# Optimization experiments

Hardware: AMD Instinct MI355X
Metric: run time of the kernel (lower is better)

Reference implementation:

```python
import jax, jax.numpy as jnp
import numpy as np

B, S, D, H = 2, 2048, 1024, 16
HD = D // H          # 64
ROT = HD // 2        # 32

def _rope(x, cos, sin):
    # x: [B,S,H,HD] -> pairs [B,S,H,ROT,2]; cos/sin: [S,ROT] -> [1,S,1,ROT]
    x2 = x.reshape(x.shape[:3] + (ROT, 2))
    x0, x1 = x2[..., 0], x2[..., 1]
    c = cos[None, :, None, :]
    s = sin[None, :, None, :]
    out = jnp.stack([x0 * c - x1 * s, x1 * c + x0 * s], axis=-1)
    return out.reshape(x.shape)

def setup_inputs() -> dict:
    key = jax.random.key(0)
    ks = jax.random.split(key, 5)
    hidden_states = jax.random.normal(ks[0], (B, S, D), dtype=jnp.float32)
    # proper rotary cos/sin table: [S, ROT, 2]
    inv_freq = 1.0 / (10000.0 ** (np.arange(0, ROT, dtype=np.float32) / ROT))
    t = np.arange(S, dtype=np.float32)
    ang = np.outer(t, inv_freq)  # [S, ROT]
    freqs = jnp.asarray(np.stack([np.cos(ang), np.sin(ang)], axis=-1), dtype=jnp.float32)
    sc = 1.0 / np.sqrt(D)
    wq = jax.random.normal(ks[1], (D, D), dtype=jnp.float32) * sc
    wk = jax.random.normal(ks[2], (D, D), dtype=jnp.float32) * sc
    wv = jax.random.normal(ks[3], (D, D), dtype=jnp.float32) * sc
    wo = jax.random.normal(ks[4], (D, D), dtype=jnp.float32) * sc
    return {"hidden_states": hidden_states, "freqs": freqs, "wq": wq, "wk": wk, "wv": wv, "wo": wo}

def reference(hidden_states, freqs, wq, wk, wv, wo):
    b, s, _ = hidden_states.shape
    scaling = HD ** -0.5
    q = (hidden_states @ wq.T).reshape(b, s, H, HD)
    k = (hidden_states @ wk.T).reshape(b, s, H, HD)
    v = (hidden_states @ wv.T).reshape(b, s, H, HD)
    cos, sin = freqs[:s, :, 0], freqs[:s, :, 1]
    q = _rope(q, cos, sin)
    k = _rope(k, cos, sin)
    # [B,H,S,S] scores, fp32 softmax
    scores = jnp.einsum('bqhd,bkhd->bhqk', q, k) * scaling
    attn = jax.nn.softmax(scores.astype(jnp.float32), axis=-1).astype(q.dtype)
    out = jnp.einsum('bhqk,bkhd->bqhd', attn, v).reshape(b, s, D)
    return out @ wo.T
```

## Files before the change

kernel.cpp:

```cpp
#include <hip/hip_runtime.h>
#include <hip/hip_bf16.h>

typedef __attribute__((ext_vector_type(8))) short bf16x8;
typedef __attribute__((ext_vector_type(4))) float f32x4;
typedef __attribute__((ext_vector_type(16))) float f32x16;
typedef __attribute__((ext_vector_type(2))) float f32x2;
typedef unsigned short u16;

#define Bc   2
#define Sc   2048
#define Dc   1024
#define Hc   16
#define HDc  64
#define ROTc 32
#define Mrows 4096

__device__ __forceinline__ u16 f2bf(float x) {
  union { float f; unsigned u; } v{x};
  unsigned r = v.u + 0x7fffu + ((v.u >> 16) & 1u);
  return (u16)(r >> 16);
}
__device__ __forceinline__ float bf2f(u16 x) {
  union { unsigned u; float f; } v{(unsigned)x << 16};
  return v.f;
}
__device__ __forceinline__ unsigned cvtpk(float a, float b) {
  unsigned r;
  asm("v_cvt_pk_bf16_f32 %0, %1, %2" : "=v"(r) : "v"(a), "v"(b));
  return r;
}
__device__ __forceinline__ f32x2 pmax2(f32x2 a, f32x2 b) {
  f32x2 r;
  r.x = fmaxf(a.x, b.x);
  r.y = fmaxf(a.y, b.y);
  return r;
}

__device__ __forceinline__ void gload_lds16(const void* g, void* l) {
  __builtin_amdgcn_global_load_lds(
      (const __attribute__((address_space(1))) void*)g,
      (__attribute__((address_space(3))) void*)l, 16, 0, 0);
}

__global__ void cvt_all(const float* __restrict__ h, const float* __restrict__ q,
                        const float* __restrict__ k, const float* __restrict__ v,
                        const float* __restrict__ o,
                        u16* __restrict__ hb, u16* __restrict__ qb, u16* __restrict__ kb,
                        u16* __restrict__ vb, u16* __restrict__ ob) {
  size_t i = ((size_t)blockIdx.x * 256 + threadIdx.x) * 4;
  const float* s;
  u16* d;
  size_t off;
  if (i < (size_t)Mrows * Dc) {
    s = h; d = hb; off = i;
  } else {
    size_t j = i - (size_t)Mrows * Dc;
    int w = (int)(j >> 20);
    off = j & ((1u << 20) - 1);
    s = (w == 0) ? q : (w == 1) ? k : (w == 2) ? v : o;
    d = (w == 0) ? qb : (w == 1) ? kb : (w == 2) ? vb : ob;
  }
  float4 val = *reinterpret_cast<const float4*>(s + off);
  u16 r0 = f2bf(val.x), r1 = f2bf(val.y), r2 = f2bf(val.z), r3 = f2bf(val.w);
  ushort4 outv = {r0, r1, r2, r3};
  *reinterpret_cast<ushort4*>(d + off) = outv;
}

__global__ void gemm_qkv(const u16* __restrict__ A, const u16* __restrict__ W0,
                         const u16* __restrict__ W1, const u16* __restrict__ W2,
                         const float* __restrict__ freqs,
                         u16* __restrict__ Qo, u16* __restrict__ Ko,
                         u16* __restrict__ Vo) {
  __shared__ u16 As[128 * 32];
  __shared__ u16 Bs[128 * 32];
  const int by = blockIdx.y;
  const int wsel = by >> 3;
  const int n0 = (by & 7) * 128;
  const int m0 = blockIdx.x * 128;
  const u16* Bm = (wsel == 0) ? W0 : (wsel == 1) ? W1 : W2;
  const int t = threadIdx.x;
  const int w = t >> 6;
  const int lane = t & 63;
  const int wm = w >> 1, wn = w & 1;
  const int c = lane & 15, g = lane >> 4;
  const int srow = t >> 2, skoff = (t & 3) * 8;

  f32x4 acc[4][4] = {};

  const u16* ag = A + (size_t)(m0 + srow) * Dc + skoff;
  const u16* bg = Bm + (size_t)(n0 + srow) * Dc + skoff;
  u16* al = &As[(w * 16) * 32];
  u16* bl = &Bs[(w * 16) * 32];

  for (int k0 = 0; k0 < Dc; k0 += 32) {
    gload_lds16(ag + k0, al);
    gload_lds16(ag + k0 + (size_t)64 * Dc, al + 64 * 32);
    gload_lds16(bg + k0, bl);
    gload_lds16(bg + k0 + (size_t)64 * Dc, bl + 64 * 32);
    __syncthreads();
    bf16x8 a[4], b[4];
#pragma unroll
    for (int f = 0; f < 4; ++f) {
      a[f] = *(const bf16x8*)&As[(wm * 64 + f * 16 + c) * 32 + g * 8];
      b[f] = *(const bf16x8*)&Bs[(wn * 64 + f * 16 + c) * 32 + g * 8];
    }
#pragma unroll
    for (int fm = 0; fm < 4; ++fm)
#pragma unroll
      for (int fn = 0; fn < 4; ++fn)
        acc[fm][fn] =
            __builtin_amdgcn_mfma_f32_16x16x32_bf16(a[fm], b[fn], acc[fm][fn], 0, 0, 0);
    __syncthreads();
  }

  u16* dst = (wsel == 0) ? Qo : (wsel == 1) ? Ko : Vo;
  const float qsc = (wsel == 0) ? 0.125f * 1.44269504f : 1.0f;
  const int codd = c & 1;
#pragma unroll
  for (int fm = 0; fm < 4; ++fm)
#pragma unroll
    for (int fn = 0; fn < 4; ++fn)
#pragma unroll
      for (int r = 0; r < 4; ++r) {
        const int m = m0 + wm * 64 + fm * 16 + g * 4 + r;
        const int n = n0 + wn * 64 + fn * 16 + c;
        float v = acc[fm][fn][r];
        const int b = m >> 11, s = m & (Sc - 1);
        const int hh = n >> 6, d = n & 63;
        size_t idx;
        if (wsel < 2) {
          const float other = __shfl_xor(v, 1);
          const float2 f = reinterpret_cast<const float2*>(freqs)[s * ROTc + (d >> 1)];
          v = codd ? (v * f.x + other * f.y) : (v * f.x - other * f.y);
          v *= qsc;
          idx = (((size_t)(b * Hc + hh) * Sc) + s) * HDc + d;
        } else {
          idx = ((size_t)(b * Hc + hh) * HDc + d) * Sc + s;
        }
        dst[idx] = f2bf(v);
      }
}

__global__ void gemm_out(const u16* __restrict__ A, const u16* __restrict__ Bm,
                         float* __restrict__ C) {
  __shared__ u16 As[64 * 32];
  __shared__ u16 Bs[128 * 32];
  const int m0 = blockIdx.x * 64;
  const int n0 = blockIdx.y * 128;
  const int t = threadIdx.x;
  const int w = t >> 6;
  const int lane = t & 63;
  const int wm = w >> 1, wn = w & 1;
  const int c = lane & 15, g = lane >> 4;
  const int srow = t >> 2, skoff = (t & 3) * 8;

  f32x4 acc[2][4] = {};

  const u16* ag = A + (size_t)(m0 + srow) * Dc + skoff;
  const u16* bg = Bm + (size_t)(n0 + srow) * Dc + skoff;
  u16* al = &As[(w * 16) * 32];
  u16* bl = &Bs[(w * 16) * 32];

  for (int k0 = 0; k0 < Dc; k0 += 32) {
    gload_lds16(ag + k0, al);
    gload_lds16(bg + k0, bl);
    gload_lds16(bg + k0 + (size_t)64 * Dc, bl + 64 * 32);
    __syncthreads();
    bf16x8 a[2], b[4];
#pragma unroll
    for (int f = 0; f < 2; ++f)
      a[f] = *(const bf16x8*)&As[(wm * 32 + f * 16 + c) * 32 + g * 8];
#pragma unroll
    for (int f = 0; f < 4; ++f)
      b[f] = *(const bf16x8*)&Bs[(wn * 64 + f * 16 + c) * 32 + g * 8];
#pragma unroll
    for (int fm = 0; fm < 2; ++fm)
#pragma unroll
      for (int fn = 0; fn < 4; ++fn)
        acc[fm][fn] =
            __builtin_amdgcn_mfma_f32_16x16x32_bf16(a[fm], b[fn], acc[fm][fn], 0, 0, 0);
    __syncthreads();
  }

#pragma unroll
  for (int fm = 0; fm < 2; ++fm)
#pragma unroll
    for (int fn = 0; fn < 4; ++fn)
#pragma unroll
      for (int r = 0; r < 4; ++r) {
        const int m = m0 + wm * 32 + fm * 16 + g * 4 + r;
        const int n = n0 + wn * 64 + fn * 16 + c;
        C[(size_t)m * Dc + n] = acc[fm][fn][r];
      }
}

__global__ __launch_bounds__(256, 2) void flash_attn(
    const u16* __restrict__ Q, const u16* __restrict__ Kb,
    const u16* __restrict__ Vt, u16* __restrict__ Ob) {
  __shared__ u16 Ks[2][32 * 128];
  __shared__ u16 Vs[2][32 * 128];
  const int orig = blockIdx.x;
  const int wg = (orig & 7) * 64 + (orig >> 3);
  const int bh = wg >> 4;
  const int q0 = (wg & 15) * 128;
  const int t = threadIdx.x, w = t >> 6, lane = t & 63;
  const int l31 = lane & 31, hi = lane >> 5;
  const int sr = t >> 4;
  const int su = (t & 15) ^ (sr & 15);
  const int skv = sr + ((su >> 3) << 5);
  const int sd8 = (su & 7) * 8;
  const int rsw = (l31 & 15);

  const u16* Qp = Q + (size_t)bh * Sc * HDc;
  const u16* Kp = Kb + (size_t)bh * Sc * HDc;
  const u16* Vp = Vt + (size_t)bh * HDc * Sc;

  const int q = q0 + w * 32 + l31;
  bf16x8 aq[4];
#pragma unroll
  for (int kd = 0; kd < 4; ++kd)
    aq[kd] = *(const bf16x8*)(Qp + (size_t)q * HDc + kd * 16 + hi * 8);

  float m_run = -1e30f, l_run = 0.f;
  f32x16 o[2] = {};

  gload_lds16(Kp + (size_t)skv * HDc + sd8, &Ks[0][w * 512]);
  gload_lds16(Kp + (size_t)(skv + 16) * HDc + sd8, &Ks[0][2048 + w * 512]);
  gload_lds16(Vp + (size_t)skv * Sc + sd8, &Vs[0][w * 512]);
  gload_lds16(Vp + (size_t)(skv + 16) * Sc + sd8, &Vs[0][2048 + w * 512]);
  __syncthreads();

  int buf = 0;
  for (int t0 = 0; t0 < Sc; t0 += 64) {
    if (t0 + 64 < Sc) {
      const int tn = t0 + 64;
      gload_lds16(Kp + (size_t)(tn + skv) * HDc + sd8, &Ks[buf ^ 1][w * 512]);
      gload_lds16(Kp + (size_t)(tn + skv + 16) * HDc + sd8, &Ks[buf ^ 1][2048 + w * 512]);
      gload_lds16(Vp + (size_t)skv * Sc + tn + sd8, &Vs[buf ^ 1][w * 512]);
      gload_lds16(Vp + (size_t)(skv + 16) * Sc + tn + sd8, &Vs[buf ^ 1][2048 + w * 512]);
    }
    f32x16 s0 = {}, s1 = {};
    __builtin_amdgcn_s_setprio(1);
#pragma unroll
    for (int kd = 0; kd < 4; ++kd) {
      const int u0 = kd * 2 + hi;
      bf16x8 a0 = *(const bf16x8*)&Ks[buf][l31 * 128 + (u0 ^ rsw) * 8];
      bf16x8 a1 = *(const bf16x8*)&Ks[buf][l31 * 128 + ((u0 + 8) ^ rsw) * 8];
      s0 = __builtin_amdgcn_mfma_f32_32x32x16_bf16(a0, aq[kd], s0, 0, 0, 0);
      s1 = __builtin_amdgcn_mfma_f32_32x32x16_bf16(a1, aq[kd], s1, 0, 0, 0);
    }
    __builtin_amdgcn_s_setprio(0);
    f32x2 t4[4];
#pragma unroll
    for (int i = 0; i < 4; ++i) {
      f32x2 e0; e0.x = s0[2 * i]; e0.y = s0[2 * i + 1];
      f32x2 e1; e1.x = s0[2 * i + 8]; e1.y = s0[2 * i + 9];
      f32x2 e2; e2.x = s1[2 * i]; e2.y = s1[2 * i + 1];
      f32x2 e3; e3.x = s1[2 * i + 8]; e3.y = s1[2 * i + 9];
      t4[i] = pmax2(pmax2(e0, e1), pmax2(e2, e3));
    }
    f32x2 tp = pmax2(pmax2(t4[0], t4[1]), pmax2(t4[2], t4[3]));
    float mt = fmaxf(tp.x, tp.y);
    mt = fmaxf(mt, __shfl_xor(mt, 32));
    const bool skip = __all(mt <= m_run + 8.0f);
    if (!skip) {
      const float mn2 = fmaxf(m_run, mt);
      const float scl = __builtin_amdgcn_exp2f(m_run - mn2);
      m_run = mn2;
      l_run *= scl;
      o[0] *= scl;
      o[1] *= scl;
    }
    const float mn = m_run;
#pragma unroll
    for (int r = 0; r < 16; ++r) {
      s0[r] = __builtin_amdgcn_exp2f(s0[r] - mn);
      s1[r] = __builtin_amdgcn_exp2f(s1[r] - mn);
    }
    f32x2 ac;
    ac.x = 0.f; ac.y = 0.f;
#pragma unroll
    for (int i = 0; i < 8; ++i) {
      f32x2 e0; e0.x = s0[2 * i]; e0.y = s0[2 * i + 1];
      f32x2 e1; e1.x = s1[2 * i]; e1.y = s1[2 * i + 1];
      ac += e0 + e1;
    }
    float rs = ac.x + ac.y;
    rs += __shfl_xor(rs, 32);
    l_run += rs;
    unsigned pk0[8], pk1[8];
#pragma unroll
    for (int B = 0; B < 4; ++B)
#pragma unroll
      for (int s2 = 0; s2 < 2; ++s2) {
        pk0[B * 2 + s2] = cvtpk(s0[4 * B + 2 * s2], s0[4 * B + 2 * s2 + 1]);
        pk1[B * 2 + s2] = cvtpk(s1[4 * B + 2 * s2], s1[4 * B + 2 * s2 + 1]);
      }
#pragma unroll
    for (int ks = 0; ks < 4; ++ks) {
      const unsigned* pk = (ks >> 1) ? pk1 : pk0;
      const int m2 = (ks & 1) * 4;
      const unsigned A0 = pk[m2 + 0], A1 = pk[m2 + 1];
      const unsigned B0 = pk[m2 + 2], B1 = pk[m2 + 3];
      const unsigned L0 = hi ? B0 : A0, L1 = hi ? B1 : A1;
      const unsigned R0 = hi ? A0 : B0, R1 = hi ? A1 : B1;
      const unsigned X0 = __shfl_xor(R0, 32), X1 = __shfl_xor(R1, 32);
      union { unsigned u[4]; bf16x8 v; } bp;
      bp.u[0] = hi ? X0 : L0;
      bp.u[1] = hi ? X1 : L1;
      bp.u[2] = hi ? L0 : X0;
      bp.u[3] = hi ? L1 : X1;
      const int uv = ks * 2 + hi;
      bf16x8 va0 = *(const bf16x8*)&Vs[buf][l31 * 128 + (uv ^ rsw) * 8];
      bf16x8 va1 = *(const bf16x8*)&Vs[buf][l31 * 128 + ((uv + 8) ^ rsw) * 8];
      __builtin_amdgcn_s_setprio(1);
      o[0] = __builtin_amdgcn_mfma_f32_32x32x16_bf16(va0, bp.v, o[0], 0, 0, 0);
      o[1] = __builtin_amdgcn_mfma_f32_32x32x16_bf16(va1, bp.v, o[1], 0, 0, 0);
      __builtin_amdgcn_s_setprio(0);
    }
    __syncthreads();
    buf ^= 1;
  }

  const float rl = 1.0f / l_run;
  const int b = bh >> 4, hh = bh & 15;
  u16* orow = Ob + ((size_t)b * Sc + q) * Dc + hh * HDc;
#pragma unroll
  for (int fv = 0; fv < 2; ++fv)
#pragma unroll
    for (int B2 = 0; B2 < 4; ++B2) {
      const float v0 = o[fv][4 * B2 + 0] * rl, v1 = o[fv][4 * B2 + 1] * rl;
      const float v2 = o[fv][4 * B2 + 2] * rl, v3 = o[fv][4 * B2 + 3] * rl;
      uint2 pv;
      pv.x = cvtpk(v0, v1);
      pv.y = cvtpk(v2, v3);
      *reinterpret_cast<uint2*>(orow + fv * 32 + 8 * B2 + 4 * hi) = pv;
    }
}

extern "C" void kernel_launch(void* const* d_in, const int* in_sizes, int n_in,
                              void* d_out, int out_size, void* d_ws, size_t ws_size,
                              hipStream_t stream) {
  (void)in_sizes; (void)n_in; (void)out_size; (void)ws_size;
  const float* hidden = (const float*)d_in[0];
  const float* freqs = (const float*)d_in[1];
  const float* wq = (const float*)d_in[2];
  const float* wk = (const float*)d_in[3];
  const float* wv = (const float*)d_in[4];
  const float* wo = (const float*)d_in[5];
  float* out = (float*)d_out;

  char* ws = (char*)d_ws;
  const size_t MB8 = (size_t)Mrows * Dc * 2;
  const size_t WB = (size_t)Dc * Dc * 2;
  u16* hb = (u16*)ws;  ws += MB8;
  u16* wqb = (u16*)ws; ws += WB;
  u16* wkb = (u16*)ws; ws += WB;
  u16* wvb = (u16*)ws; ws += WB;
  u16* wob = (u16*)ws; ws += WB;
  u16* qb = (u16*)ws;  ws += MB8;
  u16* kb = (u16*)ws;  ws += MB8;
  u16* vtb = (u16*)ws; ws += MB8;
  u16* ab = (u16*)ws;  ws += MB8;

  cvt_all<<<8192, 256, 0, stream>>>(hidden, wq, wk, wv, wo, hb, wqb, wkb, wvb, wob);
  gemm_qkv<<<dim3(32, 24), 256, 0, stream>>>(hb, wqb, wkb, wvb, freqs, qb, kb, vtb);
  flash_attn<<<512, 256, 0, stream>>>(qb, kb, vtb, ab);
  gemm_out<<<dim3(64, 8), 256, 0, stream>>>(ab, wob, out);
}
```

Before: 137.9 us.

## Software-pipeline attention loop so QK^T of next tile overlaps softmax/PV

```diff
diff --git a/kernel.cpp b/kernel.cpp
--- a/kernel.cpp
+++ b/kernel.cpp
@@ -222,41 +222,44 @@
     aq[kd] = *(const bf16x8*)(Qp + (size_t)q * HDc + kd * 16 + hi * 8);
 
   float m_run = -1e30f, l_run = 0.f;
-  f32x16 o[2] = {};
-
-  gload_lds16(Kp + (size_t)skv * HDc + sd8, &Ks[0][w * 512]);
-  gload_lds16(Kp + (size_t)(skv + 16) * HDc + sd8, &Ks[0][2048 + w * 512]);
-  gload_lds16(Vp + (size_t)skv * Sc + sd8, &Vs[0][w * 512]);
-  gload_lds16(Vp + (size_t)(skv + 16) * Sc + sd8, &Vs[0][2048 + w * 512]);
-  __syncthreads();
-
-  int buf = 0;
-  for (int t0 = 0; t0 < Sc; t0 += 64) {
-    if (t0 + 64 < Sc) {
-      const int tn = t0 + 64;
-      gload_lds16(Kp + (size_t)(tn + skv) * HDc + sd8, &Ks[buf ^ 1][w * 512]);
-      gload_lds16(Kp + (size_t)(tn + skv + 16) * HDc + sd8, &Ks[buf ^ 1][2048 + w * 512]);
-      gload_lds16(Vp + (size_t)skv * Sc + tn + sd8, &Vs[buf ^ 1][w * 512]);
-      gload_lds16(Vp + (size_t)(skv + 16) * Sc + tn + sd8, &Vs[buf ^ 1][2048 + w * 512]);
-    }
-    f32x16 s0 = {}, s1 = {};
+  f32x16 o0 = {}, o1 = {};
+  bf16x8 va0[4], va1[4];
+
+  auto STAGE = [&](int tile, int bb) {
+    const int base = tile * 64;
+    gload_lds16(Kp + (size_t)(base + skv) * HDc + sd8, &Ks[bb][w * 512]);
+    gload_lds16(Kp + (size_t)(base + skv + 16) * HDc + sd8, &Ks[bb][2048 + w * 512]);
+    gload_lds16(Vp + (size_t)skv * Sc + base + sd8, &Vs[bb][w * 512]);
+    gload_lds16(Vp + (size_t)(skv + 16) * Sc + base + sd8, &Vs[bb][2048 + w * 512]);
+  };
+  auto QKF = [&](const u16* kbase, f32x16& S0, f32x16& S1) {
     __builtin_amdgcn_s_setprio(1);
 #pragma unroll
     for (int kd = 0; kd < 4; ++kd) {
       const int u0 = kd * 2 + hi;
-      bf16x8 a0 = *(const bf16x8*)&Ks[buf][l31 * 128 + (u0 ^ rsw) * 8];
-      bf16x8 a1 = *(const bf16x8*)&Ks[buf][l31 * 128 + ((u0 + 8) ^ rsw) * 8];
-      s0 = __builtin_amdgcn_mfma_f32_32x32x16_bf16(a0, aq[kd], s0, 0, 0, 0);
-      s1 = __builtin_amdgcn_mfma_f32_32x32x16_bf16(a1, aq[kd], s1, 0, 0, 0);
+      bf16x8 a0 = *(const bf16x8*)&kbase[l31 * 128 + (u0 ^ rsw) * 8];
+      bf16x8 a1 = *(const bf16x8*)&kbase[l31 * 128 + ((u0 + 8) ^ rsw) * 8];
+      S0 = __builtin_amdgcn_mfma_f32_32x32x16_bf16(a0, aq[kd], S0, 0, 0, 0);
+      S1 = __builtin_amdgcn_mfma_f32_32x32x16_bf16(a1, aq[kd], S1, 0, 0, 0);
     }
     __builtin_amdgcn_s_setprio(0);
+  };
+  auto LOADV = [&](const u16* vbase) {
+#pragma unroll
+    for (int ks = 0; ks < 4; ++ks) {
+      const int uv = ks * 2 + hi;
+      va0[ks] = *(const bf16x8*)&vbase[l31 * 128 + (uv ^ rsw) * 8];
+      va1[ks] = *(const bf16x8*)&vbase[l31 * 128 + ((uv + 8) ^ rsw) * 8];
+    }
+  };
+  auto SMPV = [&](f32x16& S0, f32x16& S1) {
     f32x2 t4[4];
 #pragma unroll
     for (int i = 0; i < 4; ++i) {
-      f32x2 e0; e0.x = s0[2 * i]; e0.y = s0[2 * i + 1];
-      f32x2 e1; e1.x = s0[2 * i + 8]; e1.y = s0[2 * i + 9];
-      f32x2 e2; e2.x = s1[2 * i]; e2.y = s1[2 * i + 1];
-      f32x2 e3; e3.x = s1[2 * i + 8]; e3.y = s1[2 * i + 9];
+      f32x2 e0; e0.x = S0[2 * i]; e0.y = S0[2 * i + 1];
+      f32x2 e1; e1.x = S0[2 * i + 8]; e1.y = S0[2 * i + 9];
+      f32x2 e2; e2.x = S1[2 * i]; e2.y = S1[2 * i + 1];
+      f32x2 e3; e3.x = S1[2 * i + 8]; e3.y = S1[2 * i + 9];
       t4[i] = pmax2(pmax2(e0, e1), pmax2(e2, e3));
     }
     f32x2 tp = pmax2(pmax2(t4[0], t4[1]), pmax2(t4[2], t4[3]));
@@ -268,21 +271,21 @@
       const float scl = __builtin_amdgcn_exp2f(m_run - mn2);
       m_run = mn2;
       l_run *= scl;
-      o[0] *= scl;
-      o[1] *= scl;
+      o0 *= scl;
+      o1 *= scl;
     }
     const float mn = m_run;
 #pragma unroll
     for (int r = 0; r < 16; ++r) {
-      s0[r] = __builtin_amdgcn_exp2f(s0[r] - mn);
-      s1[r] = __builtin_amdgcn_exp2f(s1[r] - mn);
+      S0[r] = __builtin_amdgcn_exp2f(S0[r] - mn);
+      S1[r] = __builtin_amdgcn_exp2f(S1[r] - mn);
     }
     f32x2 ac;
     ac.x = 0.f; ac.y = 0.f;
 #pragma unroll
     for (int i = 0; i < 8; ++i) {
-      f32x2 e0; e0.x = s0[2 * i]; e0.y = s0[2 * i + 1];
-      f32x2 e1; e1.x = s1[2 * i]; e1.y = s1[2 * i + 1];
+      f32x2 e0; e0.x = S0[2 * i]; e0.y = S0[2 * i + 1];
+      f32x2 e1; e1.x = S1[2 * i]; e1.y = S1[2 * i + 1];
       ac += e0 + e1;
     }
     float rs = ac.x + ac.y;
@@ -293,9 +296,10 @@
     for (int B = 0; B < 4; ++B)
 #pragma unroll
       for (int s2 = 0; s2 < 2; ++s2) {
-        pk0[B * 2 + s2] = cvtpk(s0[4 * B + 2 * s2], s0[4 * B + 2 * s2 + 1]);
-        pk1[B * 2 + s2] = cvtpk(s1[4 * B + 2 * s2], s1[4 * B + 2 * s2 + 1]);
+        pk0[B * 2 + s2] = cvtpk(S0[4 * B + 2 * s2], S0[4 * B + 2 * s2 + 1]);
+        pk1[B * 2 + s2] = cvtpk(S1[4 * B + 2 * s2], S1[4 * B + 2 * s2 + 1]);
       }
+    bf16x8 bpv[4];
 #pragma unroll
     for (int ks = 0; ks < 4; ++ks) {
       const unsigned* pk = (ks >> 1) ? pk1 : pk0;
@@ -310,32 +314,60 @@
       bp.u[1] = hi ? X1 : L1;
       bp.u[2] = hi ? L0 : X0;
       bp.u[3] = hi ? L1 : X1;
-      const int uv = ks * 2 + hi;
-      bf16x8 va0 = *(const bf16x8*)&Vs[buf][l31 * 128 + (uv ^ rsw) * 8];
-      bf16x8 va1 = *(const bf16x8*)&Vs[buf][l31 * 128 + ((uv + 8) ^ rsw) * 8];
-      __builtin_amdgcn_s_setprio(1);
-      o[0] = __builtin_amdgcn_mfma_f32_32x32x16_bf16(va0, bp.v, o[0], 0, 0, 0);
-      o[1] = __builtin_amdgcn_mfma_f32_32x32x16_bf16(va1, bp.v, o[1], 0, 0, 0);
-      __builtin_amdgcn_s_setprio(0);
-    }
+      bpv[ks] = bp.v;
+    }
+    __builtin_amdgcn_s_setprio(1);
+#pragma unroll
+    for (int ks = 0; ks < 4; ++ks) {
+      o0 = __builtin_amdgcn_mfma_f32_32x32x16_bf16(va0[ks], bpv[ks], o0, 0, 0, 0);
+      o1 = __builtin_amdgcn_mfma_f32_32x32x16_bf16(va1[ks], bpv[ks], o1, 0, 0, 0);
+    }
+    __builtin_amdgcn_s_setprio(0);
+  };
+
+  STAGE(0, 0);
+  STAGE(1, 1);
+  __syncthreads();
+  f32x16 sp0 = {}, sp1 = {};
+  QKF(&Ks[0][0], sp0, sp1);
+  LOADV(&Vs[0][0]);
+  __syncthreads();
+
+  int buf = 1;
+  for (int tt = 1; tt < 32; ++tt) {
+    if (tt < 31) STAGE(tt + 1, buf ^ 1);
+    f32x16 sn0 = {}, sn1 = {};
+    QKF(&Ks[buf][0], sn0, sn1);
+    SMPV(sp0, sp1);
+    LOADV(&Vs[buf][0]);
     __syncthreads();
+    sp0 = sn0;
+    sp1 = sn1;
     buf ^= 1;
   }
+  SMPV(sp0, sp1);
 
   const float rl = 1.0f / l_run;
   const int b = bh >> 4, hh = bh & 15;
   u16* orow = Ob + ((size_t)b * Sc + q) * Dc + hh * HDc;
 #pragma unroll
-  for (int fv = 0; fv < 2; ++fv)
-#pragma unroll
-    for (int B2 = 0; B2 < 4; ++B2) {
-      const float v0 = o[fv][4 * B2 + 0] * rl, v1 = o[fv][4 * B2 + 1] * rl;
-      const float v2 = o[fv][4 * B2 + 2] * rl, v3 = o[fv][4 * B2 + 3] * rl;
-      uint2 pv;
-      pv.x = cvtpk(v0, v1);
-      pv.y = cvtpk(v2, v3);
-      *reinterpret_cast<uint2*>(orow + fv * 32 + 8 * B2 + 4 * hi) = pv;
-    }
+  for (int B2 = 0; B2 < 4; ++B2) {
+    const float v0 = o0[4 * B2 + 0] * rl, v1 = o0[4 * B2 + 1] * rl;
+    const float v2 = o0[4 * B2 + 2] * rl, v3 = o0[4 * B2 + 3] * rl;
+    uint2 pv;
+    pv.x = cvtpk(v0, v1);
+    pv.y = cvtpk(v2, v3);
+    *reinterpret_cast<uint2*>(orow + 8 * B2 + 4 * hi) = pv;
+  }
+#pragma unroll
+  for (int B2 = 0; B2 < 4; ++B2) {
+    const float v0 = o1[4 * B2 + 0] * rl, v1 = o1[4 * B2 + 1] * rl;
+    const float v2 = o1[4 * B2 + 2] * rl, v3 = o1[4 * B2 + 3] * rl;
+    uint2 pv;
+    pv.x = cvtpk(v0, v1);
+    pv.y = cvtpk(v2, v3);
+    *reinterpret_cast<uint2*>(orow + 32 + 8 * B2 + 4 * hi) = pv;
+  }
 }
 
 extern "C" void kernel_launch(void* const* d_in, const int* in_sizes, int n_in,
```

After: 138.5 us. No clear change (+0.4%).
